# Performance work log

Measured on AMD Instinct MI355X. Metric: run time of the kernel, lower is better.

Reference implementation:

```python
import jax, jax.numpy as jnp
import numpy as np

N_NODES = 50000
N_EDGES = 600000
IN_FEAT = 128
EDGE_DIM = 3
N_HEADS = 4
OUT_FEAT = 32  # per head; N_HEADS*OUT_FEAT == IN_FEAT -> residual_proj is Identity


def setup_inputs() -> dict:
    key = jax.random.key(0)
    ks = jax.random.split(key, 16)
    s = 0.05
    H, F = N_HEADS, OUT_FEAT
    return {
        "node_feats": jax.random.normal(ks[0], (N_NODES, IN_FEAT), jnp.float32),
        "edge_feat": jax.random.normal(ks[1], (N_EDGES, EDGE_DIM), jnp.float32),
        "src": jax.random.randint(ks[2], (N_EDGES,), 0, N_NODES),
        "dst": jax.random.randint(ks[3], (N_EDGES,), 0, N_NODES),
        "W_em1": jax.random.normal(ks[4], (EDGE_DIM, 2 * EDGE_DIM), jnp.float32) * s,
        "b_em1": jnp.zeros((2 * EDGE_DIM,), jnp.float32),
        "W_em2": jax.random.normal(ks[5], (2 * EDGE_DIM, EDGE_DIM), jnp.float32) * s,
        "b_em2": jnp.zeros((EDGE_DIM,), jnp.float32),
        "W_np": jax.random.normal(ks[6], (IN_FEAT, IN_FEAT), jnp.float32) * s,
        "b_np": jnp.zeros((IN_FEAT,), jnp.float32),
        "W_fc": jax.random.normal(ks[7], (IN_FEAT + EDGE_DIM, H * F), jnp.float32) * s,
        "attn_l": jax.random.normal(ks[8], (H, F), jnp.float32) * s,
        "attn_r": jax.random.normal(ks[9], (H, F), jnp.float32) * s,
        "gat_bias": jnp.zeros((H * F,), jnp.float32),
        "ln_gamma": jnp.ones((H * F,), jnp.float32),
        "ln_beta": jnp.zeros((H * F,), jnp.float32),
    }


def reference(node_feats, edge_feat, src, dst, W_em1, b_em1, W_em2, b_em2,
              W_np, b_np, W_fc, attn_l, attn_r, gat_bias, ln_gamma, ln_beta):
    N = node_feats.shape[0]
    H, F = attn_l.shape
    # edge MLP: Linear -> SiLU -> Linear
    e = jax.nn.silu(edge_feat @ W_em1 + b_em1) @ W_em2 + b_em2            # [E, ED]
    p = node_feats @ W_np + b_np                                          # [N, IN]
    src_in = jnp.concatenate([p[src], e], axis=1)                         # [E, IN+ED]
    dst_in = jnp.concatenate([p[dst], e], axis=1)                         # [E, IN+ED]
    temp = jnp.zeros((N, src_in.shape[1]), node_feats.dtype)
    temp = temp.at[src].add(src_in).at[dst].add(dst_in)                   # scatter_add x2
    # GATConv (eval mode: feat_drop/attn_drop are identity)
    h = (temp @ W_fc).reshape(N, H, F)                                    # [N, H, F]
    el = jnp.einsum('nhf,hf->nh', h, attn_l)                              # [N, H]
    er = jnp.einsum('nhf,hf->nh', h, attn_r)                              # [N, H]
    logits = jax.nn.leaky_relu(el[src] + er[dst], negative_slope=0.2)     # [E, H]
    # destination-wise edge softmax (stable)
    m = jax.ops.segment_max(logits, dst, num_segments=N)                  # [N, H]
    a = jnp.exp(logits - m[dst])                                          # [E, H]
    z = jax.ops.segment_sum(a, dst, num_segments=N)                       # [N, H]
    alpha = a / z[dst]                                                    # [E, H]
    msg = alpha[:, :, None] * h[src]                                      # [E, H, F]
    rst = jax.ops.segment_sum(msg, dst, num_segments=N)                   # [N, H, F]
    rst = rst + gat_bias.reshape(1, H, F)
    gat_out = rst.reshape(N, H * F)
    out = gat_out + node_feats                                            # residual (Identity proj)
    mu = out.mean(axis=-1, keepdims=True)
    var = out.var(axis=-1, keepdims=True)
    out = (out - mu) / jnp.sqrt(var + 1e-5) * ln_gamma + ln_beta          # LayerNorm
    return jax.nn.silu(out)
```

## Files before the change

### kernel.cpp

```cpp
#include <hip/hip_runtime.h>
#include <hip/hip_bf16.h>

#define IN_FEAT 128
#define N_HEADS 4
#define OUT_FEAT 32

typedef __attribute__((ext_vector_type(8))) short short8;
typedef __attribute__((ext_vector_type(4))) float floatx4;

__device__ __forceinline__ void bf16split(float x, short& hi, short& lo) {
    unsigned u = __float_as_uint(x);
    unsigned r = (u + 0x7FFFu + ((u >> 16) & 1u)) & 0xFFFF0000u;
    hi = (short)(r >> 16);
    float res = x - __uint_as_float(r);
    unsigned u2 = __float_as_uint(res);
    unsigned r2 = u2 + 0x7FFFu + ((u2 >> 16) & 1u);
    lo = (short)(r2 >> 16);
}

__device__ __forceinline__ unsigned short bf16rne(float x) {
    unsigned u = __float_as_uint(x);
    return (unsigned short)((u + 0x7FFFu + ((u >> 16) & 1u)) >> 16);
}

__global__ void edge_scatter_kernel(const float* __restrict__ ef,
                                    const int* __restrict__ src, const int* __restrict__ dst,
                                    const float* __restrict__ W1, const float* __restrict__ b1,
                                    const float* __restrict__ W2, const float* __restrict__ b2,
                                    float* __restrict__ nd, int* __restrict__ erank, int E) {
    int t = blockIdx.x * blockDim.x + threadIdx.x;
    int e = t >> 3;
    int sub = t & 7;
    if (e >= E) return;
    float x0 = ef[e * 3 + 0], x1 = ef[e * 3 + 1], x2 = ef[e * 3 + 2];
    float hbuf[6];
#pragma unroll
    for (int j = 0; j < 6; j++) {
        float v = x0 * W1[0 * 6 + j] + x1 * W1[1 * 6 + j] + x2 * W1[2 * 6 + j] + b1[j];
        hbuf[j] = v / (1.0f + __expf(-v));
    }
    int j = sub & 3;
    float val;
    if (j == 0) {
        val = 1.0f;
    } else {
        float v = b2[j - 1];
#pragma unroll
        for (int k = 0; k < 6; k++) v += hbuf[k] * W2[k * 3 + (j - 1)];
        val = v;
    }
    int side = sub >> 2;
    int node = side ? dst[e] : src[e];
    int slot = (side && j == 0) ? 4 : j;
    float old = atomicAdd(&nd[(size_t)node * 8 + slot], val);
    if (sub == 4) erank[e] = (int)old;
}

__global__ __launch_bounds__(1024) void scan1_kernel(const float* __restrict__ nd,
                                                     int* __restrict__ excl,
                                                     int* __restrict__ bsum, int N) {
    __shared__ int buf[1024];
    int t = threadIdx.x;
    int i = blockIdx.x * 1024 + t;
    int v = (i < N) ? (int)nd[(size_t)i * 8 + 4] : 0;
    buf[t] = v;
    __syncthreads();
    for (int d = 1; d < 1024; d <<= 1) {
        int x = (t >= d) ? buf[t - d] : 0;
        __syncthreads();
        buf[t] += x;
        __syncthreads();
    }
    if (i < N) excl[i] = buf[t] - v;
    if (t == 1023) bsum[blockIdx.x] = buf[1023];
}

__global__ __launch_bounds__(1024) void scan2_kernel(const int* __restrict__ bsum,
                                                     int* __restrict__ boff, int nb) {
    __shared__ int buf[1024];
    int t = threadIdx.x;
    int v = (t < nb) ? bsum[t] : 0;
    buf[t] = v;
    __syncthreads();
    for (int d = 1; d < 1024; d <<= 1) {
        int x = (t >= d) ? buf[t - d] : 0;
        __syncthreads();
        buf[t] += x;
        __syncthreads();
    }
    if (t < nb) boff[t] = buf[t] - v;
}

__global__ __launch_bounds__(1024) void scan3_kernel(const int* __restrict__ excl,
                                                     const int* __restrict__ boff,
                                                     int* __restrict__ off, int N, int E) {
    int i = blockIdx.x * 1024 + threadIdx.x;
    if (i < N) off[i] = excl[i] + boff[blockIdx.x];
    if (i == 0) off[N] = E;
}

__global__ void wcomb_kernel(const float* __restrict__ W_np, const float* __restrict__ W_fc,
                             const float* __restrict__ b_np,
                             short* __restrict__ WBh, short* __restrict__ WBl,
                             float* __restrict__ bvec) {
    int i = blockIdx.x;
    int o = threadIdx.x;
    float acc = 0.0f;
    for (int j = 0; j < 128; j++) acc += W_np[i * 128 + j] * W_fc[j * 128 + o];
    short hi, lo;
    bf16split(acc, hi, lo);
    int t    = o >> 4;
    int kk   = i >> 5;
    int lane = ((i >> 3) & 3) * 16 + (o & 15);
    int jj   = i & 7;
    int fi = ((t * 4 + kk) * 64 + lane) * 8 + jj;
    WBh[fi] = hi;
    WBl[fi] = lo;
    if (i == 0) {
        float bb = 0.0f;
        for (int j = 0; j < 128; j++) bb += b_np[j] * W_fc[j * 128 + o];
        bvec[o] = bb;
    }
}

__global__ __launch_bounds__(256) void binh_kernel(
        const int* __restrict__ src, const int* __restrict__ dst,
        const int* __restrict__ eoff, const int* __restrict__ erank,
        int* __restrict__ ssrc, int E,
        const float* __restrict__ nf,
        const short* __restrict__ WBh, const short* __restrict__ WBl,
        const float* __restrict__ bvec, const float* __restrict__ W_fc,
        const float* __restrict__ nd,
        const float* __restrict__ attn_l, const float* __restrict__ attn_r,
        unsigned short* __restrict__ h16,
        float* __restrict__ el, float* __restrict__ er, int N) {
    __shared__ short lWh[16384];
    __shared__ short lWl[16384];
    {
        const int4* s1 = (const int4*)WBh;
        const int4* s2 = (const int4*)WBl;
        int4* d1 = (int4*)lWh;
        int4* d2 = (int4*)lWl;
        for (int i = threadIdx.x; i < 2048; i += 256) { d1[i] = s1[i]; d2[i] = s2[i]; }
    }
    __syncthreads();

    {
        int stride = gridDim.x * 256;
#pragma unroll 4
        for (int e = blockIdx.x * 256 + threadIdx.x; e < E; e += stride) {
            ssrc[eoff[dst[e]] + erank[e]] = src[e];
        }
    }

    const int w = threadIdx.x >> 6, l = threadIdx.x & 63;
    const int lrow = l & 15, lhalf = l >> 4;
    const int n0 = blockIdx.x * 64 + w * 16;
    const int arow = n0 + lrow;

    short8 ah[4], al_[4];
#pragma unroll
    for (int kk = 0; kk < 4; kk++) {
        float v[8];
        if (arow < N) {
            const float* p = &nf[(size_t)arow * 128 + kk * 32 + lhalf * 8];
            float4 f0 = *(const float4*)p;
            float4 f1 = *(const float4*)(p + 4);
            v[0] = f0.x; v[1] = f0.y; v[2] = f0.z; v[3] = f0.w;
            v[4] = f1.x; v[5] = f1.y; v[6] = f1.z; v[7] = f1.w;
        } else {
#pragma unroll
            for (int j = 0; j < 8; j++) v[j] = 0.0f;
        }
#pragma unroll
        for (int j = 0; j < 8; j++) {
            short hi, lo;
            bf16split(v[j], hi, lo);
            ah[kk][j] = hi;
            al_[kk][j] = lo;
        }
    }

    floatx4 acc[8];
#pragma unroll
    for (int t = 0; t < 8; t++) acc[t] = (floatx4){0.f, 0.f, 0.f, 0.f};

#pragma unroll
    for (int t = 0; t < 8; t++) {
#pragma unroll
        for (int kk = 0; kk < 4; kk++) {
            int fi = ((t * 4 + kk) * 64 + l) * 8;
            short8 bh = *(const short8*)&lWh[fi];
            short8 bl = *(const short8*)&lWl[fi];
            acc[t] = __builtin_amdgcn_mfma_f32_16x16x32_bf16(ah[kk], bh, acc[t], 0, 0, 0);
            acc[t] = __builtin_amdgcn_mfma_f32_16x16x32_bf16(ah[kk], bl, acc[t], 0, 0, 0);
            acc[t] = __builtin_amdgcn_mfma_f32_16x16x32_bf16(al_[kk], bh, acc[t], 0, 0, 0);
        }
    }

    float bv[8], w0[8], w1[8], w2[8], alb[8], arb[8];
#pragma unroll
    for (int t = 0; t < 8; t++) {
        int o = t * 16 + lrow;
        bv[t] = bvec[o];
        w0[t] = W_fc[128 * 128 + o];
        w1[t] = W_fc[129 * 128 + o];
        w2[t] = W_fc[130 * 128 + o];
        alb[t] = attn_l[o];
        arb[t] = attn_r[o];
    }
#pragma unroll
    for (int r = 0; r < 4; r++) {
        int node = n0 + lhalf * 4 + r;
        bool valid = node < N;
        float dg = 0.f, e0 = 0.f, e1 = 0.f, e2 = 0.f;
        if (valid) {
            dg = nd[(size_t)node * 8 + 0] + nd[(size_t)node * 8 + 4];
            e0 = nd[(size_t)node * 8 + 1];
            e1 = nd[(size_t)node * 8 + 2];
            e2 = nd[(size_t)node * 8 + 3];
        }
        float pl[4] = {0.f, 0.f, 0.f, 0.f}, pr[4] = {0.f, 0.f, 0.f, 0.f};
#pragma unroll
        for (int t = 0; t < 8; t++) {
            float hv = dg * (acc[t][r] + bv[t]) + e0 * w0[t] + e1 * w1[t] + e2 * w2[t];
            if (valid) h16[(size_t)node * 128 + t * 16 + lrow] = bf16rne(hv);
            pl[t >> 1] += hv * alb[t];
            pr[t >> 1] += hv * arb[t];
        }
#pragma unroll
        for (int hd = 0; hd < 4; hd++) {
#pragma unroll
            for (int mask = 1; mask <= 8; mask <<= 1) {
                pl[hd] += __shfl_xor(pl[hd], mask);
                pr[hd] += __shfl_xor(pr[hd], mask);
            }
        }
        if (valid) {
            if (lrow < 4)      el[node * 4 + lrow]       = pl[lrow];
            else if (lrow < 8) er[node * 4 + (lrow - 4)] = pr[lrow - 4];
        }
    }
}

__global__ __launch_bounds__(256) void gather_kernel(
        const int* __restrict__ off, const int* __restrict__ sorted_src,
        const float* __restrict__ el, const float* __restrict__ er,
        const unsigned short* __restrict__ h16, const float* __restrict__ nf,
        const float* __restrict__ gat_bias, const float* __restrict__ gamma,
        const float* __restrict__ beta, float* __restrict__ out, int N) {
    int wid  = (blockIdx.x * blockDim.x + threadIdx.x) >> 6;
    int lane = threadIdx.x & 63;
    int half = lane >> 5;
    int li   = lane & 31;
    int n = wid * 2 + half;
    if (n >= N) return;
    int o0 = li * 4;
    int hd = li >> 3;
    float ern = er[(unsigned)(n * 4 + hd)];
    int beg = off[n], end = off[n + 1];
    float z = 0.f, a0 = 0.f, a1 = 0.f, a2 = 0.f, a3 = 0.f;
    if (beg < end) {
        int s = sorted_src[beg];
        float elv = el[(unsigned)(s * 4 + hd)];
        uint2 hb = *(const uint2*)&h16[(unsigned)(s * 128 + o0)];
        for (int j = beg; j < end; j++) {
            int s2 = (j + 1 < end) ? sorted_src[j + 1] : s;
            float elv2 = el[(unsigned)(s2 * 4 + hd)];
            uint2 hb2 = *(const uint2*)&h16[(unsigned)(s2 * 128 + o0)];
            float l = elv + ern;
            l = (l > 0.f) ? l : 0.2f * l;
            float p = __expf(l);
            z  += p;
            a0 += p * __uint_as_float(hb.x << 16);
            a1 += p * __uint_as_float(hb.x & 0xFFFF0000u);
            a2 += p * __uint_as_float(hb.y << 16);
            a3 += p * __uint_as_float(hb.y & 0xFFFF0000u);
            elv = elv2; hb = hb2; s = s2;
        }
    }
    float izv = (end > beg) ? 1.0f / z : 0.f;
    float4 nfv = *(const float4*)&nf[(size_t)n * 128 + o0];
    float v0 = a0 * izv + gat_bias[o0]     + nfv.x;
    float v1 = a1 * izv + gat_bias[o0 + 1] + nfv.y;
    float v2 = a2 * izv + gat_bias[o0 + 2] + nfv.z;
    float v3 = a3 * izv + gat_bias[o0 + 3] + nfv.w;
    float s  = v0 + v1 + v2 + v3;
    float s2 = v0 * v0 + v1 * v1 + v2 * v2 + v3 * v3;
#pragma unroll
    for (int mask = 1; mask <= 16; mask <<= 1) {
        s  += __shfl_xor(s, mask);
        s2 += __shfl_xor(s2, mask);
    }
    float mu = s * (1.0f / 128.0f);
    float var = s2 * (1.0f / 128.0f) - mu * mu;
    float inv = rsqrtf(var + 1e-5f);
    float y0 = (v0 - mu) * inv * gamma[o0]     + beta[o0];
    float y1 = (v1 - mu) * inv * gamma[o0 + 1] + beta[o0 + 1];
    float y2 = (v2 - mu) * inv * gamma[o0 + 2] + beta[o0 + 2];
    float y3 = (v3 - mu) * inv * gamma[o0 + 3] + beta[o0 + 3];
    float4 ov;
    ov.x = y0 / (1.0f + __expf(-y0));
    ov.y = y1 / (1.0f + __expf(-y1));
    ov.z = y2 / (1.0f + __expf(-y2));
    ov.w = y3 / (1.0f + __expf(-y3));
    *(float4*)&out[(size_t)n * 128 + o0] = ov;
}

extern "C" void kernel_launch(void* const* d_in, const int* in_sizes, int n_in,
                              void* d_out, int out_size, void* d_ws, size_t ws_size,
                              hipStream_t stream) {
    const float* nf     = (const float*)d_in[0];
    const float* ef     = (const float*)d_in[1];
    const int*   src    = (const int*)d_in[2];
    const int*   dst    = (const int*)d_in[3];
    const float* W_em1  = (const float*)d_in[4];
    const float* b_em1  = (const float*)d_in[5];
    const float* W_em2  = (const float*)d_in[6];
    const float* b_em2  = (const float*)d_in[7];
    const float* W_np   = (const float*)d_in[8];
    const float* b_np   = (const float*)d_in[9];
    const float* W_fc   = (const float*)d_in[10];
    const float* attn_l = (const float*)d_in[11];
    const float* attn_r = (const float*)d_in[12];
    const float* g_bias = (const float*)d_in[13];
    const float* ln_g   = (const float*)d_in[14];
    const float* ln_b   = (const float*)d_in[15];

    const int N = in_sizes[0] / IN_FEAT;
    const int E = in_sizes[2];

    float* ws = (float*)d_ws;
    size_t off_w = 0;
    auto alloc = [&](size_t nelem) {
        float* p = ws + off_w;
        off_w += (nelem + 63) & ~(size_t)63;
        return p;
    };
    float* nd    = alloc((size_t)N * 8);
    short* WBh   = (short*)alloc(128 * 128 / 2);
    short* WBl   = (short*)alloc(128 * 128 / 2);
    float* bvec  = alloc(128);
    unsigned short* h16 = (unsigned short*)alloc((size_t)N * 64);
    float* el    = alloc((size_t)N * 4);
    float* er    = alloc((size_t)N * 4);
    int*   erank  = (int*)alloc(E);
    int*   eoff   = (int*)alloc(N + 1);
    int*   ssrc   = (int*)alloc(E);
    int*   excl   = (int*)alloc(N);
    int*   bsum   = (int*)alloc(1024);
    int*   boff   = (int*)alloc(1024);

    const int nb = (N + 1023) / 1024;

    hipMemsetAsync(nd, 0, (size_t)N * 8 * sizeof(float), stream);

    edge_scatter_kernel<<<((size_t)E * 8 + 255) / 256, 256, 0, stream>>>(
        ef, src, dst, W_em1, b_em1, W_em2, b_em2, nd, erank, E);
    wcomb_kernel<<<128, 128, 0, stream>>>(W_np, W_fc, b_np, WBh, WBl, bvec);
    scan1_kernel<<<nb, 1024, 0, stream>>>(nd, excl, bsum, N);
    scan2_kernel<<<1, 1024, 0, stream>>>(bsum, boff, nb);
    scan3_kernel<<<nb, 1024, 0, stream>>>(excl, boff, eoff, N, E);
    binh_kernel<<<(N + 63) / 64, 256, 0, stream>>>(src, dst, eoff, erank, ssrc, E,
                                                   nf, WBh, WBl, bvec, W_fc, nd,
                                                   attn_l, attn_r, h16, el, er, N);
    gather_kernel<<<((size_t)N * 32 + 255) / 256, 256, 0, stream>>>(eoff, ssrc, el, er, h16, nf,
                                                                    g_bias, ln_g, ln_b,
                                                                    (float*)d_out, N);
}
```

Baseline: 156.5 us.

## Overlap node GEMM with edge scatter and simplify scan and finalize pipeline

```diff
diff --git a/kernel.cpp b/kernel.cpp
--- a/kernel.cpp
+++ b/kernel.cpp
@@ -23,86 +23,14 @@
     return (unsigned short)((u + 0x7FFFu + ((u >> 16) & 1u)) >> 16);
 }
 
-__global__ void edge_scatter_kernel(const float* __restrict__ ef,
-                                    const int* __restrict__ src, const int* __restrict__ dst,
-                                    const float* __restrict__ W1, const float* __restrict__ b1,
-                                    const float* __restrict__ W2, const float* __restrict__ b2,
-                                    float* __restrict__ nd, int* __restrict__ erank, int E) {
-    int t = blockIdx.x * blockDim.x + threadIdx.x;
-    int e = t >> 3;
-    int sub = t & 7;
-    if (e >= E) return;
-    float x0 = ef[e * 3 + 0], x1 = ef[e * 3 + 1], x2 = ef[e * 3 + 2];
-    float hbuf[6];
-#pragma unroll
-    for (int j = 0; j < 6; j++) {
-        float v = x0 * W1[0 * 6 + j] + x1 * W1[1 * 6 + j] + x2 * W1[2 * 6 + j] + b1[j];
-        hbuf[j] = v / (1.0f + __expf(-v));
-    }
-    int j = sub & 3;
-    float val;
-    if (j == 0) {
-        val = 1.0f;
-    } else {
-        float v = b2[j - 1];
-#pragma unroll
-        for (int k = 0; k < 6; k++) v += hbuf[k] * W2[k * 3 + (j - 1)];
-        val = v;
-    }
-    int side = sub >> 2;
-    int node = side ? dst[e] : src[e];
-    int slot = (side && j == 0) ? 4 : j;
-    float old = atomicAdd(&nd[(size_t)node * 8 + slot], val);
-    if (sub == 4) erank[e] = (int)old;
-}
-
-__global__ __launch_bounds__(1024) void scan1_kernel(const float* __restrict__ nd,
-                                                     int* __restrict__ excl,
-                                                     int* __restrict__ bsum, int N) {
-    __shared__ int buf[1024];
-    int t = threadIdx.x;
-    int i = blockIdx.x * 1024 + t;
-    int v = (i < N) ? (int)nd[(size_t)i * 8 + 4] : 0;
-    buf[t] = v;
-    __syncthreads();
-    for (int d = 1; d < 1024; d <<= 1) {
-        int x = (t >= d) ? buf[t - d] : 0;
-        __syncthreads();
-        buf[t] += x;
-        __syncthreads();
-    }
-    if (i < N) excl[i] = buf[t] - v;
-    if (t == 1023) bsum[blockIdx.x] = buf[1023];
-}
-
-__global__ __launch_bounds__(1024) void scan2_kernel(const int* __restrict__ bsum,
-                                                     int* __restrict__ boff, int nb) {
-    __shared__ int buf[1024];
-    int t = threadIdx.x;
-    int v = (t < nb) ? bsum[t] : 0;
-    buf[t] = v;
-    __syncthreads();
-    for (int d = 1; d < 1024; d <<= 1) {
-        int x = (t >= d) ? buf[t - d] : 0;
-        __syncthreads();
-        buf[t] += x;
-        __syncthreads();
-    }
-    if (t < nb) boff[t] = buf[t] - v;
-}
-
-__global__ __launch_bounds__(1024) void scan3_kernel(const int* __restrict__ excl,
-                                                     const int* __restrict__ boff,
-                                                     int* __restrict__ off, int N, int E) {
-    int i = blockIdx.x * 1024 + threadIdx.x;
-    if (i < N) off[i] = excl[i] + boff[blockIdx.x];
-    if (i == 0) off[N] = E;
-}
-
 __global__ void wcomb_kernel(const float* __restrict__ W_np, const float* __restrict__ W_fc,
                              const float* __restrict__ b_np,
                              short* __restrict__ WBh, short* __restrict__ WBl,
-                             float* __restrict__ bvec) {
+                             float* __restrict__ bvec,
+                             float4* __restrict__ ndz, int zcnt) {
+    for (int i = blockIdx.x * blockDim.x + threadIdx.x; i < zcnt; i += gridDim.x * blockDim.x)
+        ndz[i] = (float4){0.f, 0.f, 0.f, 0.f};
+
     int i = blockIdx.x;
     int o = threadIdx.x;
     float acc = 0.0f;
@@ -123,123 +51,168 @@
     }
 }
 
-__global__ __launch_bounds__(256) void binh_kernel(
+__global__ __launch_bounds__(256) void fused_kernel(
+        const float* __restrict__ ef,
+        const int* __restrict__ src, const int* __restrict__ dst,
+        const float* __restrict__ W1, const float* __restrict__ b1,
+        const float* __restrict__ W2, const float* __restrict__ b2,
+        float* __restrict__ nd, int* __restrict__ erank, int E,
+        const float* __restrict__ nf,
+        const short* __restrict__ WBh, const short* __restrict__ WBl,
+        const float* __restrict__ bvec,
+        float* __restrict__ hbase, int N, int gemmBlocks) {
+    if ((int)blockIdx.x < gemmBlocks) {
+        const int w = threadIdx.x >> 6, l = threadIdx.x & 63;
+        const int lrow = l & 15, lhalf = l >> 4;
+        const int n0 = blockIdx.x * 64 + w * 16;
+        const int arow = n0 + lrow;
+
+        short8 ah[4], al_[4];
+#pragma unroll
+        for (int kk = 0; kk < 4; kk++) {
+            float v[8];
+            if (arow < N) {
+                const float* p = &nf[(size_t)arow * 128 + kk * 32 + lhalf * 8];
+                float4 f0 = *(const float4*)p;
+                float4 f1 = *(const float4*)(p + 4);
+                v[0] = f0.x; v[1] = f0.y; v[2] = f0.z; v[3] = f0.w;
+                v[4] = f1.x; v[5] = f1.y; v[6] = f1.z; v[7] = f1.w;
+            } else {
+#pragma unroll
+                for (int j = 0; j < 8; j++) v[j] = 0.0f;
+            }
+#pragma unroll
+            for (int j = 0; j < 8; j++) {
+                short hi, lo;
+                bf16split(v[j], hi, lo);
+                ah[kk][j] = hi;
+                al_[kk][j] = lo;
+            }
+        }
+
+        const short8* gbh = (const short8*)WBh;
+        const short8* gbl = (const short8*)WBl;
+        floatx4 acc[8];
+#pragma unroll
+        for (int t = 0; t < 8; t++) acc[t] = (floatx4){0.f, 0.f, 0.f, 0.f};
+#pragma unroll
+        for (int t = 0; t < 8; t++) {
+#pragma unroll
+            for (int kk = 0; kk < 4; kk++) {
+                short8 bh = gbh[(t * 4 + kk) * 64 + l];
+                short8 bl = gbl[(t * 4 + kk) * 64 + l];
+                acc[t] = __builtin_amdgcn_mfma_f32_16x16x32_bf16(ah[kk], bh, acc[t], 0, 0, 0);
+                acc[t] = __builtin_amdgcn_mfma_f32_16x16x32_bf16(ah[kk], bl, acc[t], 0, 0, 0);
+                acc[t] = __builtin_amdgcn_mfma_f32_16x16x32_bf16(al_[kk], bh, acc[t], 0, 0, 0);
+            }
+        }
+        float bv[8];
+#pragma unroll
+        for (int t = 0; t < 8; t++) bv[t] = bvec[t * 16 + lrow];
+#pragma unroll
+        for (int r = 0; r < 4; r++) {
+            int node = n0 + lhalf * 4 + r;
+            if (node < N) {
+#pragma unroll
+                for (int t = 0; t < 8; t++)
+                    hbase[(size_t)node * 128 + t * 16 + lrow] = acc[t][r] + bv[t];
+            }
+        }
+        return;
+    }
+    int t = (blockIdx.x - gemmBlocks) * 256 + threadIdx.x;
+    int e = t >> 3;
+    int sub = t & 7;
+    if (e >= E) return;
+    float x0 = ef[e * 3 + 0], x1 = ef[e * 3 + 1], x2 = ef[e * 3 + 2];
+    float hbuf[6];
+#pragma unroll
+    for (int j = 0; j < 6; j++) {
+        float v = x0 * W1[0 * 6 + j] + x1 * W1[1 * 6 + j] + x2 * W1[2 * 6 + j] + b1[j];
+        hbuf[j] = v / (1.0f + __expf(-v));
+    }
+    int j = sub & 3;
+    float val;
+    if (j == 0) {
+        val = 1.0f;
+    } else {
+        float v = b2[j - 1];
+#pragma unroll
+        for (int k = 0; k < 6; k++) v += hbuf[k] * W2[k * 3 + (j - 1)];
+        val = v;
+    }
+    int side = sub >> 2;
+    int node = side ? dst[e] : src[e];
+    int slot = (side && j == 0) ? 4 : j;
+    float old = atomicAdd(&nd[(size_t)node * 8 + slot], val);
+    if (sub == 4) erank[e] = (int)old;
+}
+
+__global__ __launch_bounds__(1024) void scan1_kernel(const float* __restrict__ nd,
+                                                     int* __restrict__ excl,
+                                                     int* __restrict__ bsum, int N) {
+    __shared__ int buf[1024];
+    int t = threadIdx.x;
+    int i = blockIdx.x * 1024 + t;
+    int v = (i < N) ? (int)nd[(size_t)i * 8 + 4] : 0;
+    buf[t] = v;
+    __syncthreads();
+    for (int d = 1; d < 1024; d <<= 1) {
+        int x = (t >= d) ? buf[t - d] : 0;
+        __syncthreads();
+        buf[t] += x;
+        __syncthreads();
+    }
+    if (i < N) excl[i] = buf[t] - v;
+    if (t == 1023) bsum[blockIdx.x] = buf[1023];
+}
+
+__global__ __launch_bounds__(1024) void scan3_kernel(const int* __restrict__ excl,
+                                                     const int* __restrict__ bsum,
+                                                     int* __restrict__ off, int N, int E) {
+    __shared__ int base;
+    if (threadIdx.x == 0) {
+        int s = 0;
+        for (int k = 0; k < (int)blockIdx.x; k++) s += bsum[k];
+        base = s;
+    }
+    __syncthreads();
+    int i = blockIdx.x * 1024 + threadIdx.x;
+    if (i < N) off[i] = excl[i] + base;
+    if (i == 0) off[N] = E;
+}
+
+__global__ __launch_bounds__(256) void finalize_kernel(
         const int* __restrict__ src, const int* __restrict__ dst,
         const int* __restrict__ eoff, const int* __restrict__ erank,
         int* __restrict__ ssrc, int E,
-        const float* __restrict__ nf,
-        const short* __restrict__ WBh, const short* __restrict__ WBl,
-        const float* __restrict__ bvec, const float* __restrict__ W_fc,
-        const float* __restrict__ nd,
+        const float* __restrict__ hbase, const float* __restrict__ nd,
+        const float* __restrict__ W_fc,
         const float* __restrict__ attn_l, const float* __restrict__ attn_r,
         unsigned short* __restrict__ h16,
         float* __restrict__ el, float* __restrict__ er, int N) {
-    __shared__ short lWh[16384];
-    __shared__ short lWl[16384];
-    {
-        const int4* s1 = (const int4*)WBh;
-        const int4* s2 = (const int4*)WBl;
-        int4* d1 = (int4*)lWh;
-        int4* d2 = (int4*)lWl;
-        for (int i = threadIdx.x; i < 2048; i += 256) { d1[i] = s1[i]; d2[i] = s2[i]; }
-    }
-    __syncthreads();
-
-    {
-        int stride = gridDim.x * 256;
-#pragma unroll 4
-        for (int e = blockIdx.x * 256 + threadIdx.x; e < E; e += stride) {
-            ssrc[eoff[dst[e]] + erank[e]] = src[e];
-        }
-    }
-
-    const int w = threadIdx.x >> 6, l = threadIdx.x & 63;
-    const int lrow = l & 15, lhalf = l >> 4;
-    const int n0 = blockIdx.x * 64 + w * 16;
-    const int arow = n0 + lrow;
-
-    short8 ah[4], al_[4];
-#pragma unroll
-    for (int kk = 0; kk < 4; kk++) {
-        float v[8];
-        if (arow < N) {
-            const float* p = &nf[(size_t)arow * 128 + kk * 32 + lhalf * 8];
-            float4 f0 = *(const float4*)p;
-            float4 f1 = *(const float4*)(p + 4);
-            v[0] = f0.x; v[1] = f0.y; v[2] = f0.z; v[3] = f0.w;
-            v[4] = f1.x; v[5] = f1.y; v[6] = f1.z; v[7] = f1.w;
-        } else {
-#pragma unroll
-            for (int j = 0; j < 8; j++) v[j] = 0.0f;
-        }
-#pragma unroll
-        for (int j = 0; j < 8; j++) {
-            short hi, lo;
-            bf16split(v[j], hi, lo);
-            ah[kk][j] = hi;
-            al_[kk][j] = lo;
-        }
-    }
-
-    floatx4 acc[8];
-#pragma unroll
-    for (int t = 0; t < 8; t++) acc[t] = (floatx4){0.f, 0.f, 0.f, 0.f};
-
-#pragma unroll
-    for (int t = 0; t < 8; t++) {
-#pragma unroll
-        for (int kk = 0; kk < 4; kk++) {
-            int fi = ((t * 4 + kk) * 64 + l) * 8;
-            short8 bh = *(const short8*)&lWh[fi];
-            short8 bl = *(const short8*)&lWl[fi];
-            acc[t] = __builtin_amdgcn_mfma_f32_16x16x32_bf16(ah[kk], bh, acc[t], 0, 0, 0);
-            acc[t] = __builtin_amdgcn_mfma_f32_16x16x32_bf16(ah[kk], bl, acc[t], 0, 0, 0);
-            acc[t] = __builtin_amdgcn_mfma_f32_16x16x32_bf16(al_[kk], bh, acc[t], 0, 0, 0);
-        }
-    }
-
-    float bv[8], w0[8], w1[8], w2[8], alb[8], arb[8];
-#pragma unroll
-    for (int t = 0; t < 8; t++) {
-        int o = t * 16 + lrow;
-        bv[t] = bvec[o];
-        w0[t] = W_fc[128 * 128 + o];
-        w1[t] = W_fc[129 * 128 + o];
-        w2[t] = W_fc[130 * 128 + o];
-        alb[t] = attn_l[o];
-        arb[t] = attn_r[o];
-    }
-#pragma unroll
-    for (int r = 0; r < 4; r++) {
-        int node = n0 + lhalf * 4 + r;
-        bool valid = node < N;
-        float dg = 0.f, e0 = 0.f, e1 = 0.f, e2 = 0.f;
-        if (valid) {
-            dg = nd[(size_t)node * 8 + 0] + nd[(size_t)node * 8 + 4];
-            e0 = nd[(size_t)node * 8 + 1];
-            e1 = nd[(size_t)node * 8 + 2];
-            e2 = nd[(size_t)node * 8 + 3];
-        }
-        float pl[4] = {0.f, 0.f, 0.f, 0.f}, pr[4] = {0.f, 0.f, 0.f, 0.f};
-#pragma unroll
-        for (int t = 0; t < 8; t++) {
-            float hv = dg * (acc[t][r] + bv[t]) + e0 * w0[t] + e1 * w1[t] + e2 * w2[t];
-            if (valid) h16[(size_t)node * 128 + t * 16 + lrow] = bf16rne(hv);
-            pl[t >> 1] += hv * alb[t];
-            pr[t >> 1] += hv * arb[t];
-        }
-#pragma unroll
-        for (int hd = 0; hd < 4; hd++) {
-#pragma unroll
-            for (int mask = 1; mask <= 8; mask <<= 1) {
-                pl[hd] += __shfl_xor(pl[hd], mask);
-                pr[hd] += __shfl_xor(pr[hd], mask);
-            }
-        }
-        if (valid) {
-            if (lrow < 4)      el[node * 4 + lrow]       = pl[lrow];
-            else if (lrow < 8) er[node * 4 + (lrow - 4)] = pr[lrow - 4];
-        }
+    int gtid = blockIdx.x * 256 + threadIdx.x;
+    if (gtid < E) ssrc[eoff[dst[gtid]] + erank[gtid]] = src[gtid];
+
+    int node = blockIdx.x * 2 + (threadIdx.x >> 7);
+    if (node >= N) return;
+    int o = threadIdx.x & 127;
+    float hb = hbase[(size_t)node * 128 + o];
+    float dg = nd[node * 8 + 0] + nd[node * 8 + 4];
+    float hv = dg * hb
+             + nd[node * 8 + 1] * W_fc[128 * 128 + o]
+             + nd[node * 8 + 2] * W_fc[129 * 128 + o]
+             + nd[node * 8 + 3] * W_fc[130 * 128 + o];
+    h16[(size_t)node * 128 + o] = bf16rne(hv);
+    float pl = hv * attn_l[o], pr = hv * attn_r[o];
+#pragma unroll
+    for (int mask = 1; mask <= 16; mask <<= 1) {
+        pl += __shfl_xor(pl, mask);
+        pr += __shfl_xor(pr, mask);
+    }
+    if ((o & 31) == 0) {
+        el[node * 4 + (o >> 5)] = pl;
+        er[node * 4 + (o >> 5)] = pr;
     }
 }
 
@@ -341,6 +314,7 @@
     short* WBh   = (short*)alloc(128 * 128 / 2);
     short* WBl   = (short*)alloc(128 * 128 / 2);
     float* bvec  = alloc(128);
+    float* hbase = alloc((size_t)N * 128);
     unsigned short* h16 = (unsigned short*)alloc((size_t)N * 64);
     float* el    = alloc((size_t)N * 4);
     float* er    = alloc((size_t)N * 4);
@@ -349,21 +323,21 @@
     int*   ssrc   = (int*)alloc(E);
     int*   excl   = (int*)alloc(N);
     int*   bsum   = (int*)alloc(1024);
-    int*   boff   = (int*)alloc(1024);
 
     const int nb = (N + 1023) / 1024;
-
-    hipMemsetAsync(nd, 0, (size_t)N * 8 * sizeof(float), stream);
-
-    edge_scatter_kernel<<<((size_t)E * 8 + 255) / 256, 256, 0, stream>>>(
-        ef, src, dst, W_em1, b_em1, W_em2, b_em2, nd, erank, E);
-    wcomb_kernel<<<128, 128, 0, stream>>>(W_np, W_fc, b_np, WBh, WBl, bvec);
+    const int gemmBlocks = (N + 63) / 64;
+    const int scatBlocks = ((size_t)E * 8 + 255) / 256;
+
+    wcomb_kernel<<<128, 128, 0, stream>>>(W_np, W_fc, b_np, WBh, WBl, bvec,
+                                          (float4*)nd, N * 2);
+    fused_kernel<<<gemmBlocks + scatBlocks, 256, 0, stream>>>(
+        ef, src, dst, W_em1, b_em1, W_em2, b_em2, nd, erank, E,
+        nf, WBh, WBl, bvec, hbase, N, gemmBlocks);
     scan1_kernel<<<nb, 1024, 0, stream>>>(nd, excl, bsum, N);
-    scan2_kernel<<<1, 1024, 0, stream>>>(bsum, boff, nb);
-    scan3_kernel<<<nb, 1024, 0, stream>>>(excl, boff, eoff, N, E);
-    binh_kernel<<<(N + 63) / 64, 256, 0, stream>>>(src, dst, eoff, erank, ssrc, E,
-                                                   nf, WBh, WBl, bvec, W_fc, nd,
-                                                   attn_l, attn_r, h16, el, er, N);
+    scan3_kernel<<<nb, 1024, 0, stream>>>(excl, bsum, eoff, N, E);
+    finalize_kernel<<<(N + 1) / 2, 256, 0, stream>>>(src, dst, eoff, erank, ssrc, E,
+                                                     hbase, nd, W_fc, attn_l, attn_r,
+                                                     h16, el, er, N);
     gather_kernel<<<((size_t)N * 32 + 255) / 256, 256, 0, stream>>>(eoff, ssrc, el, er, h16, nf,
                                                                     g_bias, ln_g, ln_b,
                                                                     (float*)d_out, N);
```

Result: faster. 149.4 us (-4.6%).
